# Performance work log

Hardware: AMD Instinct MI355X
Metric: run time of the kernel (lower is better)

Reference implementation:

```python
import jax, jax.numpy as jnp
from jax import lax
import numpy as np

N, C, H, W = 16, 128, 128, 128
CH = C // 4  # adapter contraction channels


def setup_inputs() -> dict:
    key = jax.random.key(0)
    ks = jax.random.split(key, 12)
    x = jax.random.normal(ks[0], (N, C, H, W), jnp.float32)
    # intensity in {1,2,3} as the torch module expects (intensity[i]-1 indexes adapters)
    intensity = jax.random.randint(ks[1], (N,), 1, 4)
    conv1_w = jax.random.normal(ks[2], (C, C, 3, 3), jnp.float32) * 0.02
    conv1_b = jnp.zeros((C,), jnp.float32)
    prelu1 = jnp.float32(0.25)  # nn.PReLU default single shared slope
    conv2_w = jax.random.normal(ks[3], (C, C, 3, 3), jnp.float32) * 0.02
    conv2_b = jnp.zeros((C,), jnp.float32)
    # 3 adapter experts, stacked on leading axis
    aW1 = jax.random.normal(ks[4], (3, CH, C), jnp.float32) * 0.05
    ab1 = jnp.zeros((3, CH), jnp.float32)
    aW2 = jax.random.normal(ks[5], (3, C, CH), jnp.float32) * 0.05
    ab2 = jnp.zeros((3, C), jnp.float32)
    prelu2 = jnp.float32(0.25)
    return dict(x=x, intensity=intensity, conv1_w=conv1_w, conv1_b=conv1_b,
                prelu1=prelu1, conv2_w=conv2_w, conv2_b=conv2_b,
                aW1=aW1, ab1=ab1, aW2=aW2, ab2=ab2, prelu2=prelu2)


def prelu(x, a):
    return jnp.where(x >= 0, x, a * x)


def conv3x3(x, w, b):
    y = lax.conv_general_dilated(x, w, window_strides=(1, 1),
                                 padding=((1, 1), (1, 1)),
                                 dimension_numbers=('NCHW', 'OIHW', 'NCHW'))
    return y + b[None, :, None, None]


def reference(x, intensity, conv1_w, conv1_b, prelu1, conv2_w, conv2_b,
              aW1, ab1, aW2, ab2, prelu2):
    h = prelu(conv3x3(x, conv1_w, conv1_b), prelu1)      # conv1 + PReLU
    h = conv3x3(h, conv2_w, conv2_b)                     # conv2, no activation
    x1 = jnp.mean(h, axis=(2, 3))                        # AdaptiveAvgPool2d(1)+Flatten -> [N,C]
    idx = intensity - 1                                  # expert id per sample
    W1, b1 = aW1[idx], ab1[idx]                          # gather per-sample expert weights
    W2, b2 = aW2[idx], ab2[idx]
    a = jax.nn.relu(jnp.einsum('nc,nhc->nh', x1, W1) + b1)
    g = jnp.einsum('nh,nch->nc', a, W2) + b2             # [N,C]
    out = h * jax.nn.sigmoid(g)[:, :, None, None] + x    # gated residual
    return prelu(out, prelu2)
```

## Files before the change

### kernel.cpp

```cpp
#include <hip/hip_runtime.h>
#include <hip/hip_bf16.h>
#include <math.h>

#define NN   16
#define C_   128
#define HH   128
#define WW   128
#define CHID 32
#define NTILES 64

typedef short bf16x8 __attribute__((ext_vector_type(8)));
typedef float f32x4  __attribute__((ext_vector_type(4)));

__device__ inline void glds16(const void* g, void* l) {
    __builtin_amdgcn_global_load_lds(
        (const __attribute__((address_space(1))) unsigned int*)g,
        (__attribute__((address_space(3))) unsigned int*)l, 16, 0, 0);
}

__device__ inline unsigned short f2bf(float f) {
    __hip_bfloat16 h = __float2bfloat16(f);
    return *reinterpret_cast<unsigned short*>(&h);
}

__global__ __launch_bounds__(64) void pack_w_k(
    const float* __restrict__ w1, const float* __restrict__ w2,
    unsigned short* __restrict__ wl)
{
    const int b = blockIdx.x;
    const int conv = b / 288, rem = b % 288;
    const int kk = rem / 32, ck = (rem % 32) / 8, cot = rem % 8;
    const int l = threadIdx.x;
    const int co  = cot * 16 + (l & 15);
    const int ci0 = ck * 32 + (l >> 4) * 8;
    const float* W = conv ? w2 : w1;
    union { unsigned short u[8]; uint4 v; } pk;
#pragma unroll
    for (int j = 0; j < 8; ++j)
        pk.u[j] = f2bf(W[(size_t)(co * C_ + ci0 + j) * 9 + kk]);
    unsigned short* dst = wl + (size_t)conv * 147456 +
        ((((size_t)kk * 4 + ck) * 8 + cot) * 64 + l) * 8;
    *reinterpret_cast<uint4*>(dst) = pk.v;
}

__global__ __launch_bounds__(256) void to_cnhwc_k(
    const float* __restrict__ x, unsigned short* __restrict__ xb)
{
    __shared__ unsigned short s_t[128][136];
    const int y = blockIdx.x, n = blockIdx.y, t = threadIdx.x;

#pragma unroll
    for (int p = 0; p < 16; ++p) {
        int fi = p * 256 + t;
        int ci = fi >> 5, x0 = (fi & 31) * 4;
        float4 v = *reinterpret_cast<const float4*>(
            x + (((size_t)(n * C_ + ci) * HH) + y) * WW + x0);
        const int slot = ((ci >> 3) ^ ((x0 >> 2) & 7)) * 8 + (ci & 7);
        s_t[x0 + 0][slot] = f2bf(v.x);
        s_t[x0 + 1][slot] = f2bf(v.y);
        s_t[x0 + 2][slot] = f2bf(v.z);
        s_t[x0 + 3][slot] = f2bf(v.w);
    }
    __syncthreads();
    unsigned short* dstbase = xb + ((size_t)(n * HH + y)) * 16384;
#pragma unroll
    for (int p = 0; p < 8; ++p) {
        int o = p * 256 + t;
        int ck = o >> 9, u = o & 511;
        int xc = u >> 2, q = u & 3;
        int k = ck * 4 + q;
        uint4 v = *reinterpret_cast<const uint4*>(
            &s_t[xc][(k ^ ((xc >> 2) & 7)) * 8]);
        *reinterpret_cast<uint4*>(dstbase + (size_t)ck * 4096 + xc * 32 + q * 8) = v;
    }
}

template<int CONV>
__global__ __launch_bounds__(512) void conv_mfma_k(
    const unsigned short* __restrict__ inb,
    const unsigned short* __restrict__ wl,
    const float* __restrict__ bias,
    const float* __restrict__ prelu_a,
    unsigned short* __restrict__ outb,
    float* __restrict__ outf,
    float* __restrict__ partial)
{
    __shared__ char  smem[34816];
    __shared__ float s_part[8][64];

    const int tid = threadIdx.x;
    const int l = tid & 63, w = tid >> 6;
    const int wco = w >> 2, wy = (w >> 1) & 1, wxh = w & 1;
    const int lg = l >> 4, l15 = l & 15;
    const int yp = blockIdx.x, n = blockIdx.z;
    const int y0 = yp * 2;

    const f32x4 fz = {0.f, 0.f, 0.f, 0.f};
    f32x4 acc[4][4];
#pragma unroll
    for (int m = 0; m < 4; ++m)
#pragma unroll
        for (int nf = 0; nf < 4; ++nf) acc[m][nf] = fz;

    const bf16x8* wv = reinterpret_cast<const bf16x8*>(wl);
    char* sb0 = smem;
    const uint4 z4 = {0u, 0u, 0u, 0u};

    for (int ck = 0; ck < 4; ++ck) {
        __syncthreads();
        {
            const int r = w >> 1, xh = w & 1;
            const int ygl = y0 - 1 + r;
            if (ygl < 0 || ygl >= HH) {
                int t2 = xh * 64 + l;
                for (int i = t2; i < 528; i += 128)
                    *reinterpret_cast<uint4*>(sb0 + r * 8448 + i * 16) = z4;
            } else {
                if (xh == 0 && l < 8) {
                    int col = (l < 4) ? 0 : 129, q = l & 3;
                    *reinterpret_cast<uint4*>(sb0 + r * 8448 + col * 64 + q * 16) = z4;
                }
                size_t rowbase = (((size_t)(n * HH + ygl)) * 4 + ck) * 8192;
#pragma unroll
                for (int i = 0; i < 4; ++i) {
                    const int p  = xh * 64 + i * 16 + (l >> 2);
                    const int sd = (l & 3) ^ (((1 + p) >> 1) & 3);
                    const char* g = (const char*)inb + rowbase + (size_t)p * 64 + sd * 16;
                    glds16(g, sb0 + r * 8448 + (1 + xh * 64 + i * 16) * 64);
                }
            }
        }
        __syncthreads();

        bf16x8 a_cur[4];
#pragma unroll
        for (int m = 0; m < 4; ++m)
            a_cur[m] = wv[(((size_t)0 * 4 + ck) * 8 + wco * 4 + m) * 64 + l];

#pragma unroll
        for (int kk = 0; kk < 9; ++kk) {
            const int ky = kk / 3, kx = kk % 3;
            bf16x8 a_nxt[4];
            if (kk < 8) {
#pragma unroll
                for (int m = 0; m < 4; ++m)
                    a_nxt[m] = wv[((((size_t)kk + 1) * 4 + ck) * 8 + wco * 4 + m) * 64 + l];
            }
            const int rrow = wy + ky;
            bf16x8 b[4];
#pragma unroll
            for (int nf = 0; nf < 4; ++nf) {
                int xi = wxh * 64 + nf * 16 + l15 + kx;
                int slot = lg ^ ((xi >> 1) & 3);
                b[nf] = *reinterpret_cast<const bf16x8*>(
                    sb0 + rrow * 8448 + xi * 64 + slot * 16);
            }
#pragma unroll
            for (int nf = 0; nf < 4; ++nf)
#pragma unroll
                for (int m = 0; m < 4; ++m)
                    acc[m][nf] = __builtin_amdgcn_mfma_f32_16x16x32_bf16(
                        a_cur[m], b[nf], acc[m][nf], 0, 0, 0);
            if (kk < 8) {
#pragma unroll
                for (int m = 0; m < 4; ++m) a_cur[m] = a_nxt[m];
            }
        }
    }

    const int ybase = y0 + wy;
    if (CONV == 1) {
        const float a1 = *prelu_a;
        unsigned short (*s_rp)[136] = reinterpret_cast<unsigned short (*)[136]>(smem);
        for (int r = 0; r < 2; ++r) {
            __syncthreads();
            if (wy == r) {
#pragma unroll
                for (int m = 0; m < 4; ++m) {
                    const int co0 = wco * 64 + m * 16 + lg * 4;
#pragma unroll
                    for (int nf = 0; nf < 4; ++nf) {
                        const int xc = wxh * 64 + nf * 16 + l15;
                        union { unsigned short u[4]; uint2 v; } pk;
#pragma unroll
                        for (int jj = 0; jj < 4; ++jj) {
                            float f = acc[m][nf][jj] + bias[co0 + jj];
                            f = (f >= 0.f) ? f : a1 * f;
                            pk.u[jj] = f2bf(f);
                        }
                        *reinterpret_cast<uint2*>(&s_rp[xc][co0]) = pk.v;
                    }
                }
            }
            __syncthreads();
            const int y = y0 + r;
#pragma unroll
            for (int p = 0; p < 4; ++p) {
                int u = p * 512 + tid;
                int xc = u >> 4, k = u & 15;
                uint4 v = *reinterpret_cast<const uint4*>(&s_rp[xc][k * 8]);
                *reinterpret_cast<uint4*>(outb +
                    (((size_t)(n * HH + y)) * 4 + (k >> 2)) * 4096 +
                    xc * 32 + (k & 3) * 8) = v;
            }
        }
    } else {
        float ps[4][4];
#pragma unroll
        for (int m = 0; m < 4; ++m)
#pragma unroll
            for (int jj = 0; jj < 4; ++jj) ps[m][jj] = 0.f;
#pragma unroll
        for (int m = 0; m < 4; ++m) {
            const int co0 = wco * 64 + m * 16 + lg * 4;
#pragma unroll
            for (int nf = 0; nf < 4; ++nf) {
                const int xc = wxh * 64 + nf * 16 + l15;
#pragma unroll
                for (int jj = 0; jj < 4; ++jj) {
                    float f = acc[m][nf][jj] + bias[co0 + jj];
                    outf[(((size_t)(n * C_ + co0 + jj)) * HH + ybase) * WW + xc] = f;
                    ps[m][jj] += f;
                }
            }
        }
#pragma unroll
        for (int m = 0; m < 4; ++m)
#pragma unroll
            for (int jj = 0; jj < 4; ++jj) {
                float s = ps[m][jj];
                s += __shfl_xor(s, 1); s += __shfl_xor(s, 2);
                s += __shfl_xor(s, 4); s += __shfl_xor(s, 8);
                ps[m][jj] = s;
            }
        if (l15 == 0) {
#pragma unroll
            for (int m = 0; m < 4; ++m)
#pragma unroll
                for (int jj = 0; jj < 4; ++jj)
                    s_part[w][m * 16 + lg * 4 + jj] = ps[m][jj];
        }
        __syncthreads();
        if (tid < C_) {
            const int half = tid >> 6;
            float s = 0.f;
#pragma unroll
            for (int w2 = 0; w2 < 4; ++w2) s += s_part[half * 4 + w2][tid & 63];
            partial[((size_t)(n * C_ + tid)) * NTILES + yp] = s;
        }
    }
}

__global__ __launch_bounds__(C_) void adapter_k(
    const float* __restrict__ partial, const int* __restrict__ intensity,
    const float* __restrict__ aW1, const float* __restrict__ ab1,
    const float* __restrict__ aW2, const float* __restrict__ ab2,
    float* __restrict__ sig)
{
    __shared__ float sx[C_];
    __shared__ float sa[CHID];
    const int n = blockIdx.x, c = threadIdx.x;

    float s = 0.f;
    for (int t = 0; t < NTILES; ++t)
        s += partial[(size_t)(n * C_ + c) * NTILES + t];
    sx[c] = s * (1.f / (float)(HH * WW));
    __syncthreads();

    const int idx = intensity[n] - 1;
    if (c < CHID) {
        float a = ab1[idx * CHID + c];
        const float* wrow = aW1 + (size_t)(idx * CHID + c) * C_;
        for (int k = 0; k < C_; ++k) a = fmaf(wrow[k], sx[k], a);
        sa[c] = fmaxf(a, 0.f);
    }
    __syncthreads();

    float g = ab2[idx * C_ + c];
    const float* w2row = aW2 + (size_t)(idx * C_ + c) * CHID;
#pragma unroll
    for (int k = 0; k < CHID; ++k) g = fmaf(w2row[k], sa[k], g);
    sig[n * C_ + c] = 1.f / (1.f + expf(-g));
}

__global__ __launch_bounds__(256) void epilogue_k(
    const float* __restrict__ x, const float* __restrict__ sig,
    const float* __restrict__ prelu_a, float* __restrict__ out, int total4)
{
    const float a = *prelu_a;
    const int stride = gridDim.x * blockDim.x;
    for (int i = blockIdx.x * blockDim.x + threadIdx.x; i < total4; i += stride) {
        const int nc = (i * 4) >> 14;
        const float s = sig[nc];
        float4 h4 = ((const float4*)out)[i];
        float4 x4 = ((const float4*)x)[i];
        float4 v;
        v.x = h4.x * s + x4.x;  v.x = (v.x >= 0.f) ? v.x : a * v.x;
        v.y = h4.y * s + x4.y;  v.y = (v.y >= 0.f) ? v.y : a * v.y;
        v.z = h4.z * s + x4.z;  v.z = (v.z >= 0.f) ? v.z : a * v.z;
        v.w = h4.w * s + x4.w;  v.w = (v.w >= 0.f) ? v.w : a * v.w;
        ((float4*)out)[i] = v;
    }
}

extern "C" void kernel_launch(void* const* d_in, const int* in_sizes, int n_in,
                              void* d_out, int out_size, void* d_ws, size_t ws_size,
                              hipStream_t stream)
{
    const float* x         = (const float*)d_in[0];
    const int*   intensity = (const int*)  d_in[1];
    const float* w1        = (const float*)d_in[2];
    const float* b1        = (const float*)d_in[3];
    const float* p1        = (const float*)d_in[4];
    const float* w2        = (const float*)d_in[5];
    const float* b2        = (const float*)d_in[6];
    const float* aW1       = (const float*)d_in[7];
    const float* ab1       = (const float*)d_in[8];
    const float* aW2       = (const float*)d_in[9];
    const float* ab2       = (const float*)d_in[10];
    const float* p2        = (const float*)d_in[11];
    float* out = (float*)d_out;

    unsigned short* xb = (unsigned short*)d_out;

    unsigned short* h1b = (unsigned short*)d_ws;
    unsigned short* wl  = (unsigned short*)((char*)d_ws + (size_t)33554432 * 2);
    float* partial = (float*)((char*)wl + (size_t)294912 * 2);
    float* sig     = partial + (size_t)NN * C_ * NTILES;

    pack_w_k<<<dim3(576), dim3(64), 0, stream>>>(w1, w2, wl);
    to_cnhwc_k<<<dim3(HH, NN), dim3(256), 0, stream>>>(x, xb);

    conv_mfma_k<1><<<dim3(NTILES, 1, NN), dim3(512), 0, stream>>>(
        xb, wl, b1, p1, h1b, nullptr, nullptr);
    conv_mfma_k<2><<<dim3(NTILES, 1, NN), dim3(512), 0, stream>>>(
        h1b, wl + (size_t)147456, b2, nullptr, nullptr, out, partial);

    adapter_k<<<dim3(NN), dim3(C_), 0, stream>>>(
        partial, intensity, aW1, ab1, aW2, ab2, sig);

    const int total4 = NN * C_ * HH * WW / 4;
    epilogue_k<<<dim3(2048), dim3(256), 0, stream>>>(x, sig, p2, out, total4);
}
```

Before: 275.3 us.

## Switch conv MFMA to 32x32x16 tiles with double-buffered half-chunk LDS staging

Replaces the 16x16x32 bf16 MFMA tiling with 32x32x16 instructions, repacking weights into 16-channel K chunks and reshaping the accumulators, epilogue and partial-sum reductions to match. Input staging now loads 16-channel half chunks into two LDS buffers, so the next chunk's global-to-LDS copy overlaps the current chunk's MFMAs. This cuts barrier stalls and per-MFMA operand loads, at the cost of more loop iterations and a new swizzle and epilogue layout that must stay correct.

```diff
diff --git a/kernel.cpp b/kernel.cpp
--- a/kernel.cpp
+++ b/kernel.cpp
@@ -9,8 +9,11 @@
 #define CHID 32
 #define NTILES 64
 
+#define ROWB 4160
+#define HC   16640
+
 typedef short bf16x8 __attribute__((ext_vector_type(8)));
-typedef float f32x4  __attribute__((ext_vector_type(4)));
+typedef float f32x16 __attribute__((ext_vector_type(16)));
 
 __device__ inline void glds16(const void* g, void* l) {
     __builtin_amdgcn_global_load_lds(
@@ -29,17 +32,17 @@
 {
     const int b = blockIdx.x;
     const int conv = b / 288, rem = b % 288;
-    const int kk = rem / 32, ck = (rem % 32) / 8, cot = rem % 8;
+    const int kk = rem / 32, ck8 = (rem % 32) / 4, cot = rem % 4;
     const int l = threadIdx.x;
-    const int co  = cot * 16 + (l & 15);
-    const int ci0 = ck * 32 + (l >> 4) * 8;
+    const int co  = cot * 32 + (l & 31);
+    const int ci0 = ck8 * 16 + (l >> 5) * 8;
     const float* W = conv ? w2 : w1;
     union { unsigned short u[8]; uint4 v; } pk;
 #pragma unroll
     for (int j = 0; j < 8; ++j)
         pk.u[j] = f2bf(W[(size_t)(co * C_ + ci0 + j) * 9 + kk]);
     unsigned short* dst = wl + (size_t)conv * 147456 +
-        ((((size_t)kk * 4 + ck) * 8 + cot) * 64 + l) * 8;
+        ((((size_t)kk * 8 + ck8) * 4 + cot) * 64 + l) * 8;
     *reinterpret_cast<uint4*>(dst) = pk.v;
 }
 
@@ -91,81 +94,89 @@
     const int tid = threadIdx.x;
     const int l = tid & 63, w = tid >> 6;
     const int wco = w >> 2, wy = (w >> 1) & 1, wxh = w & 1;
-    const int lg = l >> 4, l15 = l & 15;
+    const int l31 = l & 31, sel = l >> 5;
     const int yp = blockIdx.x, n = blockIdx.z;
     const int y0 = yp * 2;
 
-    const f32x4 fz = {0.f, 0.f, 0.f, 0.f};
-    f32x4 acc[4][4];
-#pragma unroll
-    for (int m = 0; m < 4; ++m)
-#pragma unroll
-        for (int nf = 0; nf < 4; ++nf) acc[m][nf] = fz;
+    f32x16 acc[2][2];
+#pragma unroll
+    for (int m = 0; m < 2; ++m)
+#pragma unroll
+        for (int nf = 0; nf < 2; ++nf)
+#pragma unroll
+            for (int r = 0; r < 16; ++r) acc[m][nf][r] = 0.f;
 
     const bf16x8* wv = reinterpret_cast<const bf16x8*>(wl);
-    char* sb0 = smem;
     const uint4 z4 = {0u, 0u, 0u, 0u};
 
-    for (int ck = 0; ck < 4; ++ck) {
-        __syncthreads();
-        {
-            const int r = w >> 1, xh = w & 1;
+    auto stage = [&](int ck8, char* buf) {
+        const int ck = ck8 >> 1, h2 = (ck8 & 1) * 2;
+        if (tid < 16) {
+            int r = tid >> 2, xi = (tid & 2) ? 129 : 0, sl = tid & 1;
+            *reinterpret_cast<uint4*>(buf + r * ROWB + xi * 32 + sl * 16) = z4;
+        }
+#pragma unroll
+        for (int j = 0; j < 2; ++j) {
+            const int ub = j * 512 + w * 64;
+            const int r  = ub >> 8;
+            char* ldst = buf + r * ROWB + 32 + (ub & 255) * 16;
             const int ygl = y0 - 1 + r;
+            const int u  = ub + l;
+            const int xi = 1 + ((u & 255) >> 1), sl = u & 1;
             if (ygl < 0 || ygl >= HH) {
-                int t2 = xh * 64 + l;
-                for (int i = t2; i < 528; i += 128)
-                    *reinterpret_cast<uint4*>(sb0 + r * 8448 + i * 16) = z4;
+                *reinterpret_cast<uint4*>(ldst + l * 16) = z4;
             } else {
-                if (xh == 0 && l < 8) {
-                    int col = (l < 4) ? 0 : 129, q = l & 3;
-                    *reinterpret_cast<uint4*>(sb0 + r * 8448 + col * 64 + q * 16) = z4;
-                }
-                size_t rowbase = (((size_t)(n * HH + ygl)) * 4 + ck) * 8192;
-#pragma unroll
-                for (int i = 0; i < 4; ++i) {
-                    const int p  = xh * 64 + i * 16 + (l >> 2);
-                    const int sd = (l & 3) ^ (((1 + p) >> 1) & 3);
-                    const char* g = (const char*)inb + rowbase + (size_t)p * 64 + sd * 16;
-                    glds16(g, sb0 + r * 8448 + (1 + xh * 64 + i * 16) * 64);
-                }
-            }
-        }
-        __syncthreads();
-
-        bf16x8 a_cur[4];
-#pragma unroll
-        for (int m = 0; m < 4; ++m)
-            a_cur[m] = wv[(((size_t)0 * 4 + ck) * 8 + wco * 4 + m) * 64 + l];
+                const int o = h2 + (sl ^ ((xi >> 2) & 1));
+                const char* g = (const char*)inb +
+                    (((size_t)(n * HH + ygl)) * 4 + ck) * 8192 +
+                    (size_t)(xi - 1) * 64 + o * 16;
+                glds16(g, ldst);
+            }
+        }
+    };
+
+    stage(0, smem);
+    __syncthreads();
+
+    for (int ck8 = 0; ck8 < 8; ++ck8) {
+        char* buf = smem + (ck8 & 1) * HC;
+        if (ck8 < 7) stage(ck8 + 1, smem + ((ck8 + 1) & 1) * HC);
+
+        bf16x8 a_cur[2];
+#pragma unroll
+        for (int m = 0; m < 2; ++m)
+            a_cur[m] = wv[(((0 * 8 + ck8) * 4) + wco * 2 + m) * 64 + l];
 
 #pragma unroll
         for (int kk = 0; kk < 9; ++kk) {
             const int ky = kk / 3, kx = kk % 3;
-            bf16x8 a_nxt[4];
+            bf16x8 a_nxt[2];
             if (kk < 8) {
 #pragma unroll
-                for (int m = 0; m < 4; ++m)
-                    a_nxt[m] = wv[((((size_t)kk + 1) * 4 + ck) * 8 + wco * 4 + m) * 64 + l];
+                for (int m = 0; m < 2; ++m)
+                    a_nxt[m] = wv[((((kk + 1) * 8 + ck8) * 4) + wco * 2 + m) * 64 + l];
             }
             const int rrow = wy + ky;
-            bf16x8 b[4];
-#pragma unroll
-            for (int nf = 0; nf < 4; ++nf) {
-                int xi = wxh * 64 + nf * 16 + l15 + kx;
-                int slot = lg ^ ((xi >> 1) & 3);
+            bf16x8 b[2];
+#pragma unroll
+            for (int nf = 0; nf < 2; ++nf) {
+                const int xi = wxh * 64 + nf * 32 + l31 + kx;
+                const int sl = sel ^ ((xi >> 2) & 1);
                 b[nf] = *reinterpret_cast<const bf16x8*>(
-                    sb0 + rrow * 8448 + xi * 64 + slot * 16);
-            }
-#pragma unroll
-            for (int nf = 0; nf < 4; ++nf)
-#pragma unroll
-                for (int m = 0; m < 4; ++m)
-                    acc[m][nf] = __builtin_amdgcn_mfma_f32_16x16x32_bf16(
+                    buf + rrow * ROWB + xi * 32 + sl * 16);
+            }
+#pragma unroll
+            for (int nf = 0; nf < 2; ++nf)
+#pragma unroll
+                for (int m = 0; m < 2; ++m)
+                    acc[m][nf] = __builtin_amdgcn_mfma_f32_32x32x16_bf16(
                         a_cur[m], b[nf], acc[m][nf], 0, 0, 0);
             if (kk < 8) {
 #pragma unroll
-                for (int m = 0; m < 4; ++m) a_cur[m] = a_nxt[m];
-            }
-        }
+                for (int m = 0; m < 2; ++m) a_cur[m] = a_nxt[m];
+            }
+        }
+        __syncthreads();
     }
 
     const int ybase = y0 + wy;
@@ -173,24 +184,25 @@
         const float a1 = *prelu_a;
         unsigned short (*s_rp)[136] = reinterpret_cast<unsigned short (*)[136]>(smem);
         for (int r = 0; r < 2; ++r) {
-            __syncthreads();
             if (wy == r) {
 #pragma unroll
-                for (int m = 0; m < 4; ++m) {
-                    const int co0 = wco * 64 + m * 16 + lg * 4;
-#pragma unroll
-                    for (int nf = 0; nf < 4; ++nf) {
-                        const int xc = wxh * 64 + nf * 16 + l15;
-                        union { unsigned short u[4]; uint2 v; } pk;
-#pragma unroll
-                        for (int jj = 0; jj < 4; ++jj) {
-                            float f = acc[m][nf][jj] + bias[co0 + jj];
-                            f = (f >= 0.f) ? f : a1 * f;
-                            pk.u[jj] = f2bf(f);
+                for (int m = 0; m < 2; ++m)
+#pragma unroll
+                    for (int nf = 0; nf < 2; ++nf) {
+                        const int xc = wxh * 64 + nf * 32 + l31;
+#pragma unroll
+                        for (int q = 0; q < 4; ++q) {
+                            const int co0 = wco * 64 + m * 32 + q * 8 + sel * 4;
+                            union { unsigned short u[4]; uint2 v; } pk;
+#pragma unroll
+                            for (int jj = 0; jj < 4; ++jj) {
+                                float f = acc[m][nf][q * 4 + jj] + bias[co0 + jj];
+                                f = (f >= 0.f) ? f : a1 * f;
+                                pk.u[jj] = f2bf(f);
+                            }
+                            *reinterpret_cast<uint2*>(&s_rp[xc][co0]) = pk.v;
                         }
-                        *reinterpret_cast<uint2*>(&s_rp[xc][co0]) = pk.v;
                     }
-                }
             }
             __syncthreads();
             const int y = y0 + r;
@@ -203,42 +215,48 @@
                     (((size_t)(n * HH + y)) * 4 + (k >> 2)) * 4096 +
                     xc * 32 + (k & 3) * 8) = v;
             }
+            __syncthreads();
         }
     } else {
-        float ps[4][4];
-#pragma unroll
-        for (int m = 0; m < 4; ++m)
-#pragma unroll
-            for (int jj = 0; jj < 4; ++jj) ps[m][jj] = 0.f;
-#pragma unroll
-        for (int m = 0; m < 4; ++m) {
-            const int co0 = wco * 64 + m * 16 + lg * 4;
-#pragma unroll
-            for (int nf = 0; nf < 4; ++nf) {
-                const int xc = wxh * 64 + nf * 16 + l15;
-#pragma unroll
-                for (int jj = 0; jj < 4; ++jj) {
-                    float f = acc[m][nf][jj] + bias[co0 + jj];
-                    outf[(((size_t)(n * C_ + co0 + jj)) * HH + ybase) * WW + xc] = f;
-                    ps[m][jj] += f;
+        float ps[2][16];
+#pragma unroll
+        for (int m = 0; m < 2; ++m)
+#pragma unroll
+            for (int r = 0; r < 16; ++r) ps[m][r] = 0.f;
+#pragma unroll
+        for (int m = 0; m < 2; ++m)
+#pragma unroll
+            for (int nf = 0; nf < 2; ++nf) {
+                const int x = wxh * 64 + nf * 32 + l31;
+#pragma unroll
+                for (int q = 0; q < 4; ++q) {
+                    const int co0 = wco * 64 + m * 32 + q * 8 + sel * 4;
+#pragma unroll
+                    for (int jj = 0; jj < 4; ++jj) {
+                        float f = acc[m][nf][q * 4 + jj] + bias[co0 + jj];
+                        outf[(((size_t)(n * C_ + co0 + jj)) * HH + ybase) * WW + x] = f;
+                        ps[m][q * 4 + jj] += f;
+                    }
                 }
             }
-        }
-#pragma unroll
-        for (int m = 0; m < 4; ++m)
-#pragma unroll
-            for (int jj = 0; jj < 4; ++jj) {
-                float s = ps[m][jj];
-                s += __shfl_xor(s, 1); s += __shfl_xor(s, 2);
-                s += __shfl_xor(s, 4); s += __shfl_xor(s, 8);
-                ps[m][jj] = s;
-            }
-        if (l15 == 0) {
-#pragma unroll
-            for (int m = 0; m < 4; ++m)
-#pragma unroll
-                for (int jj = 0; jj < 4; ++jj)
-                    s_part[w][m * 16 + lg * 4 + jj] = ps[m][jj];
+#pragma unroll
+        for (int m = 0; m < 2; ++m)
+#pragma unroll
+            for (int r = 0; r < 16; ++r) {
+                float s = ps[m][r];
+                s += __shfl_xor(s, 1);  s += __shfl_xor(s, 2);
+                s += __shfl_xor(s, 4);  s += __shfl_xor(s, 8);
+                s += __shfl_xor(s, 16);
+                ps[m][r] = s;
+            }
+        if (l31 == 0) {
+#pragma unroll
+            for (int m = 0; m < 2; ++m)
+#pragma unroll
+                for (int q = 0; q < 4; ++q)
+#pragma unroll
+                    for (int jj = 0; jj < 4; ++jj)
+                        s_part[w][m * 32 + q * 8 + sel * 4 + jj] = ps[m][q * 4 + jj];
         }
         __syncthreads();
         if (tid < C_) {
```

Result: slower. 350.0 us (+27.2%).
